# Kernel optimization log

Measured on AMD Instinct MI355X. Metric: run time of the kernel, lower is better.

Reference implementation:

```python
import jax, jax.numpy as jnp
import numpy as np

K = 1024          # num_embeddings (static for segment_sum)
D = 256           # embedding_dim
B, H, W = 32, 64, 64
DECAY = 0.99
EPS = 1e-05
BETA = 0.25


def setup_inputs() -> dict:
    key = jax.random.key(0)
    k1, k2 = jax.random.split(key)
    z = jax.random.normal(k1, (B, D, H, W), dtype=jnp.float32)
    embedding = jax.random.normal(k2, (K, D), dtype=jnp.float32)
    ema_cluster_size = jnp.zeros((K,), dtype=jnp.float32)
    ema_embedding = embedding.copy()
    return {"z": z, "embedding": embedding,
            "ema_cluster_size": ema_cluster_size,
            "ema_embedding": ema_embedding}


def reference(z, embedding, ema_cluster_size, ema_embedding):
    b, d, h, w = z.shape
    # (B, D, H, W) -> (B*H*W, D)
    z_flat = jnp.transpose(z, (0, 2, 3, 1)).reshape(-1, d)
    # squared L2 distances to each code: ||z||^2 - 2 z.E^T + ||E||^2  -> (N, K)
    dist = (jnp.sum(z_flat * z_flat, axis=1, keepdims=True)
            - 2.0 * (z_flat @ embedding.T)
            + jnp.sum(embedding * embedding, axis=1))
    encoding_indices = jnp.argmin(dist, axis=1)                 # (N,)
    # one-hot @ embedding == gather
    quantized = embedding[encoding_indices]                     # (N, D)
    quantized = jnp.transpose(quantized.reshape(b, h, w, d), (0, 3, 1, 2))
    # EMA buffer updates (encodings.sum(0) and encodings.T @ z_flat as segment sums)
    counts = jax.ops.segment_sum(jnp.ones_like(encoding_indices, dtype=z.dtype),
                                 encoding_indices, num_segments=K)
    dw = jax.ops.segment_sum(z_flat, encoding_indices, num_segments=K)
    new_cluster_size = DECAY * ema_cluster_size + (1.0 - DECAY) * counts
    new_ema_embedding = DECAY * ema_embedding + (1.0 - DECAY) * dw
    # straight-through estimator
    quantized_ste = z + jax.lax.stop_gradient(quantized - z)
    commitment_loss = BETA * jnp.mean(jnp.square(z - jax.lax.stop_gradient(quantized_ste)))
    return (quantized_ste, commitment_loss, encoding_indices,
            new_cluster_size, new_ema_embedding)
```

## Files before the change

### kernel.cpp

```cpp
#include <hip/hip_runtime.h>

#define KC 1024
#define DD 256
#define NP 131072
#define HWSZ 4096
#define TOTZ 33554432

#define OUT_Q    0
#define OUT_LOSS 33554432
#define OUT_IDX  33554433
#define OUT_CS   33685505
#define OUT_EMA  33686529

#define WS_IDX    0
#define WS_COUNTS 131072
#define WS_RCNT   132096
#define WS_LOSSP  132352
#define WS_ENORM  132608
#define WS_RLIST  133632
#define WS_EAUG   264704
#define WS_ZAUG   657920
#define WS_NEED_FLOATS (WS_ZAUG + 33554432)

#define MARGIN 0.0625f
#define RTILE 16

typedef __attribute__((ext_vector_type(8))) short bf16x8;
typedef __attribute__((ext_vector_type(4))) float f32x4;

__device__ inline unsigned short f2bf_rne(float x) {
    unsigned u = __float_as_uint(x);
    unsigned r = u + 0x7FFFu + ((u >> 16) & 1u);
    return (unsigned short)(r >> 16);
}
__device__ inline float bf2f(unsigned short h) {
    return __uint_as_float(((unsigned)h) << 16);
}
__device__ inline void gl_lds16(const void* g, void* l) {
    __builtin_amdgcn_global_load_lds(
        (const __attribute__((address_space(1))) unsigned int*)g,
        (__attribute__((address_space(3))) unsigned int*)l, 16, 0, 0);
}
__device__ inline unsigned long long packkey(float d, int c) {
    unsigned u = __float_as_uint(d);
    u = (u & 0x80000000u) ? ~u : (u | 0x80000000u);
    return (((unsigned long long)u) << 32) | (unsigned)c;
}

__global__ __launch_bounds__(256) void enorm_kernel(const float* __restrict__ emb,
                                                    float* __restrict__ enorm) {
    const int k = blockIdx.x;
    float v = emb[k * DD + threadIdx.x];
    v *= v;
    #pragma unroll
    for (int off = 32; off > 0; off >>= 1) v += __shfl_down(v, off);
    __shared__ float red[4];
    if ((threadIdx.x & 63) == 0) red[threadIdx.x >> 6] = v;
    __syncthreads();
    if (threadIdx.x == 0) enorm[k] = (red[0] + red[1]) + (red[2] + red[3]);
}

__global__ __launch_bounds__(256) void convert_z_kernel(
    const float* __restrict__ z, unsigned short* __restrict__ zaug)
{
    const int blk = blockIdx.x;
    const int pt = blk >> 2, kslot = blk & 3;
    const int kbase0 = kslot * 64;
    unsigned short* outH = zaug + (size_t)(pt * 8 + kslot) * 8192;
    unsigned short* outM = zaug + (size_t)(pt * 8 + 4 + kslot) * 8192;
    #pragma unroll
    for (int i = 0; i < 4; ++i) {
        const int f = i * 256 + threadIdx.x;
        const int kc = f >> 9, mt = (f >> 6) & 7, lane = f & 63;
        const int q = lane >> 4, col = lane & 15;
        const int p = pt * 128 + mt * 16 + col;
        const int b = p >> 12, hw = p & 4095;
        const int k0 = kbase0 + kc * 32 + q * 8;
        const float* src = z + (size_t)b * 1048576 + (size_t)k0 * 4096 + hw;
        unsigned short vh[8], vm[8];
        #pragma unroll
        for (int j = 0; j < 8; ++j) {
            const float x = src[j * 4096];
            const unsigned short h = f2bf_rne(x);
            vh[j] = h;
            vm[j] = f2bf_rne(x - bf2f(h));
        }
        *(uint4*)(outH + (size_t)f * 8) = *(uint4*)vh;
        *(uint4*)(outM + (size_t)f * 8) = *(uint4*)vm;
    }
}

__global__ __launch_bounds__(256) void convert_emb_kernel(
    const float* __restrict__ emb, unsigned short* __restrict__ eaug)
{
    const int blk = blockIdx.x;
    const int cc = blk / 12, ks = blk % 12;
    const int mode = (ks >= 8);
    unsigned short* outp = eaug + (size_t)blk * 8192;
    #pragma unroll
    for (int i = 0; i < 4; ++i) {
        const int f = i * 256 + threadIdx.x;
        const int kc = f >> 9, nt = (f >> 6) & 7, lane = f & 63;
        const int q = lane >> 4, col = lane & 15;
        const int n = cc * 128 + nt * 16 + col;
        const int k0 = ((ks * 64) & 255) + kc * 32 + q * 8;
        const float* src = emb + (size_t)n * 256 + k0;
        unsigned short v[8];
        #pragma unroll
        for (int j = 0; j < 8; ++j) {
            const float x = src[j];
            const unsigned short h = f2bf_rne(x);
            v[j] = mode ? f2bf_rne(x - bf2f(h)) : h;
        }
        *(uint4*)(outp + (size_t)f * 8) = *(uint4*)v;
    }
}

__global__ __launch_bounds__(512) void gemm_argmin_kernel(
    const unsigned short* __restrict__ zaug, const unsigned short* __restrict__ eaug,
    const float* __restrict__ enorm, int* __restrict__ idx_out,
    float* __restrict__ idx_out_f, float* __restrict__ counts,
    int* __restrict__ rcnt, int* __restrict__ rlist)
{
    __shared__ float smem[12288];
    unsigned short* aS   = (unsigned short*)smem;
    unsigned short* bAll = aS + 8192;
    const int t = threadIdx.x, w = t >> 6, lane = t & 63;
    const int w2 = w & 3, cho = w >> 2;
    const int mh = w2 & 1, nh = w2 >> 1;
    const int pt = blockIdx.x;

    const int aoff = w * 1024 + lane * 8;
    const int boff = w * 2048 + lane * 8;

    float rb[16], rs[16]; int ri[16];
    #pragma unroll
    for (int s = 0; s < 16; ++s) { rb[s] = 3.4e38f; rs[s] = 3.4e38f; ri[s] = 0; }

    #pragma unroll 1
    for (int pp = 0; pp < 4; ++pp) {
        const int cc = pp * 2 + cho;
        f32x4 acc[4][4];
        #pragma unroll
        for (int mi = 0; mi < 4; ++mi)
            #pragma unroll
            for (int ni = 0; ni < 4; ++ni) acc[mi][ni] = (f32x4){0.f, 0.f, 0.f, 0.f};

        float en[4];
        #pragma unroll
        for (int ni = 0; ni < 4; ++ni)
            en[ni] = enorm[cc * 128 + nh * 64 + ni * 16 + (lane & 15)];

        #pragma unroll 1
        for (int ks = 0; ks < 12; ++ks) {
            const int ksA = (ks < 8) ? ks : (ks - 8);
            const unsigned short* ga = zaug + ((size_t)(pt * 8 + ksA)) * 8192;
            const unsigned short* gbase = (w < 4)
                ? eaug + ((size_t)((pp * 2 + 0) * 12 + ks)) * 8192
                : eaug + ((size_t)((pp * 2 + 1) * 12 + ks)) * 8192 - 8192;
            __syncthreads();
            gl_lds16(ga + aoff, aS + aoff);
            gl_lds16(ga + aoff + 512, aS + aoff + 512);
            #pragma unroll
            for (int j = 0; j < 4; ++j)
                gl_lds16(gbase + boff + j * 512, bAll + boff + j * 512);
            __syncthreads();
            #pragma unroll
            for (int kc = 0; kc < 2; ++kc) {
                bf16x8 af[4], bf[4];
                #pragma unroll
                for (int mi = 0; mi < 4; ++mi)
                    af[mi] = *(const bf16x8*)(aS + kc * 4096 + (mh * 4 + mi) * 512 + lane * 8);
                #pragma unroll
                for (int ni = 0; ni < 4; ++ni)
                    bf[ni] = *(const bf16x8*)(bAll + cho * 8192 + kc * 4096 + (nh * 4 + ni) * 512 + lane * 8);
                #pragma unroll
                for (int mi = 0; mi < 4; ++mi)
                    #pragma unroll
                    for (int ni = 0; ni < 4; ++ni)
                        acc[mi][ni] = __builtin_amdgcn_mfma_f32_16x16x32_bf16(
                            af[mi], bf[ni], acc[mi][ni], 0, 0, 0);
            }
        }
        #pragma unroll
        for (int mi = 0; mi < 4; ++mi) {
            #pragma unroll
            for (int r = 0; r < 4; ++r) {
                const int s = mi * 4 + r;
                float v0 = fmaf(-2.f, acc[mi][0][r], en[0]);
                float v1 = fmaf(-2.f, acc[mi][1][r], en[1]);
                float v2 = fmaf(-2.f, acc[mi][2][r], en[2]);
                float v3 = fmaf(-2.f, acc[mi][3][r], en[3]);
                const int nb = cc * 128 + nh * 64 + (lane & 15);
                float b01 = fminf(v0, v1), x01 = fmaxf(v0, v1);
                int   i01 = (v1 < v0) ? nb + 16 : nb;
                float b23 = fminf(v2, v3), x23 = fmaxf(v2, v3);
                int   i23 = (v3 < v2) ? nb + 48 : nb + 32;
                float b = fminf(b01, b23);
                int   ib = (b23 < b01) ? i23 : i01;
                float s2 = fminf(fmaxf(b01, b23), fminf(x01, x23));
                if (b < rb[s]) { rs[s] = fminf(rb[s], s2); rb[s] = b; ri[s] = ib; }
                else           { rs[s] = fminf(rs[s], b); }
            }
        }
    }

    float B = 3.4e38f, S = 3.4e38f; int I = 0;
    const int mi_f = (t >> 4) & 3, q_f = (t >> 2) & 3, r_f = t & 3;
    const int s_f = mi_f * 4 + r_f;
    #pragma unroll 1
    for (int phase = 0; phase < 2; ++phase) {
        __syncthreads();
        if (cho == phase) {
            #pragma unroll
            for (int s = 0; s < 16; ++s) {
                smem[w2 * 1024 + s * 64 + lane] = rb[s];
                smem[4096 + w2 * 1024 + s * 64 + lane] = rs[s];
                ((int*)smem)[8192 + w2 * 1024 + s * 64 + lane] = ri[s];
            }
        }
        __syncthreads();
        if (t < 128) {
            #pragma unroll
            for (int hh = 0; hh < 2; ++hh) {
                const int wv = (t >> 6) + hh * 2;
                const int base = wv * 1024 + s_f * 64 + q_f * 16;
                #pragma unroll
                for (int ln = 0; ln < 16; ++ln) {
                    const float b = smem[base + ln];
                    const float s2 = smem[4096 + base + ln];
                    const int   i = ((int*)smem)[8192 + base + ln];
                    if (b < B) { S = fminf(B, s2); B = b; I = i; }
                    else       { S = fminf(S, b); }
                }
            }
        }
    }
    if (t < 128) {
        const int p = pt * 128 + t;
        idx_out[p] = I;
        idx_out_f[p] = (float)I;
        atomicAdd(&counts[I], 1.0f);
        if (S - B < MARGIN) {
            const int pos = atomicAdd(rcnt, 1);
            rlist[pos] = p;
        }
    }
}

__global__ __launch_bounds__(256) void rescue_kernel(
    const float* __restrict__ z, const float* __restrict__ emb,
    const float* __restrict__ enorm, const int* __restrict__ rcnt,
    const int* __restrict__ rlist, int* __restrict__ idx_out,
    float* __restrict__ idx_out_f, float* __restrict__ counts)
{
    __shared__ float zl[RTILE][DD];
    __shared__ unsigned long long lkey[RTILE];
    const int n = *rcnt;
    if (n <= 0) return;
    const int ntiles = (n + RTILE - 1) / RTILE;
    const int t = threadIdx.x;
    const int slot = t & 15, drow = t >> 4;
    #pragma unroll 1
    for (int tile = blockIdx.x; tile < ntiles; tile += gridDim.x) {
        const int base = tile * RTILE;
        {
            const int ridx = min(base + slot, n - 1);
            const int p = rlist[ridx];
            const int b = p >> 12, hw = p & 4095;
            const float* zp = z + (size_t)b * 1048576 + hw;
            #pragma unroll
            for (int j = 0; j < 16; ++j)
                zl[slot][drow * 16 + j] = zp[(size_t)(drow * 16 + j) * 4096];
        }
        if (t < RTILE) lkey[t] = ~0ull;
        __syncthreads();
        float dot[RTILE][4];
        #pragma unroll
        for (int p = 0; p < RTILE; ++p)
            #pragma unroll
            for (int ci = 0; ci < 4; ++ci) dot[p][ci] = 0.f;
        #pragma unroll 1
        for (int d4 = 0; d4 < 64; ++d4) {
            float4 ev[4];
            #pragma unroll
            for (int ci = 0; ci < 4; ++ci)
                ev[ci] = *(const float4*)(emb + (size_t)(ci * 256 + t) * 256 + d4 * 4);
            #pragma unroll
            for (int p = 0; p < RTILE; ++p) {
                const float4 zv = *(const float4*)(&zl[p][d4 * 4]);
                #pragma unroll
                for (int ci = 0; ci < 4; ++ci) {
                    dot[p][ci] = fmaf(zv.x, ev[ci].x, dot[p][ci]);
                    dot[p][ci] = fmaf(zv.y, ev[ci].y, dot[p][ci]);
                    dot[p][ci] = fmaf(zv.z, ev[ci].z, dot[p][ci]);
                    dot[p][ci] = fmaf(zv.w, ev[ci].w, dot[p][ci]);
                }
            }
        }
        float en[4];
        #pragma unroll
        for (int ci = 0; ci < 4; ++ci) en[ci] = enorm[ci * 256 + t];
        #pragma unroll
        for (int p = 0; p < RTILE; ++p) {
            unsigned long long k = packkey(fmaf(-2.f, dot[p][0], en[0]), t);
            #pragma unroll
            for (int ci = 1; ci < 4; ++ci) {
                const unsigned long long k2 =
                    packkey(fmaf(-2.f, dot[p][ci], en[ci]), ci * 256 + t);
                k = (k2 < k) ? k2 : k;
            }
            atomicMin(&lkey[p], k);
        }
        __syncthreads();
        if (t < RTILE && base + t < n) {
            const int p = rlist[base + t];
            const int fc = (int)(lkey[t] & 0xFFFFFFFFull);
            const int old = idx_out[p];
            if (fc != old) {
                atomicAdd(&counts[old], -1.0f);
                atomicAdd(&counts[fc], 1.0f);
                idx_out[p] = fc;
                idx_out_f[p] = (float)fc;
            }
        }
        __syncthreads();
    }
}

__global__ __launch_bounds__(512) void dwq_kernel(
    const float* __restrict__ z, const float* __restrict__ emb,
    const int* __restrict__ idx, const float* __restrict__ ema_emb,
    float* __restrict__ out_q, float* __restrict__ out_ema,
    float* __restrict__ lossp)
{
    __shared__ float kdw[KC];
    __shared__ float ecol[KC];
    __shared__ float red[8];
    const int d = blockIdx.x;
    const int t = threadIdx.x;
    #pragma unroll
    for (int k = t; k < KC; k += 512) { kdw[k] = 0.f; ecol[k] = emb[(size_t)k * 256 + d]; }
    __syncthreads();
    float ls = 0.f;
    #pragma unroll 1
    for (int it = 0; it < 64; ++it) {
        const int e = it * 512 + t;
        const int b = e >> 10, hwi = (e & 1023) << 2;
        const size_t zoff = (size_t)b * 1048576 + (size_t)d * 4096 + hwi;
        const float4 zv = *(const float4*)(z + zoff);
        const int4 iv = *(const int4*)(idx + b * 4096 + hwi);
        const float q0 = ecol[iv.x], q1 = ecol[iv.y], q2 = ecol[iv.z], q3 = ecol[iv.w];
        float4 qv; qv.x = q0; qv.y = q1; qv.z = q2; qv.w = q3;
        *(float4*)(out_q + zoff) = qv;
        atomicAdd(&kdw[iv.x], zv.x);
        atomicAdd(&kdw[iv.y], zv.y);
        atomicAdd(&kdw[iv.z], zv.z);
        atomicAdd(&kdw[iv.w], zv.w);
        const float d0 = zv.x - q0, d1 = zv.y - q1, d2 = zv.z - q2, d3 = zv.w - q3;
        ls += (d0 * d0 + d1 * d1) + (d2 * d2 + d3 * d3);
    }
    __syncthreads();
    #pragma unroll
    for (int k = t; k < KC; k += 512)
        out_ema[(size_t)k * 256 + d] = 0.99f * ema_emb[(size_t)k * 256 + d] + 0.01f * kdw[k];
    #pragma unroll
    for (int off = 32; off > 0; off >>= 1) ls += __shfl_down(ls, off);
    if ((t & 63) == 0) red[t >> 6] = ls;
    __syncthreads();
    if (t == 0) {
        float s = 0.f;
        #pragma unroll
        for (int i = 0; i < 8; ++i) s += red[i];
        lossp[blockIdx.x] = s;
    }
}

__global__ __launch_bounds__(256) void finalize_kernel(
    const float* __restrict__ ema_cs, const float* __restrict__ counts,
    const float* __restrict__ lossp, float* __restrict__ out)
{
    const int i = blockIdx.x * 256 + threadIdx.x;
    out[OUT_CS + i] = 0.99f * ema_cs[i] + 0.01f * counts[i];
    if (blockIdx.x == 0) {
        float s = lossp[threadIdx.x];
        #pragma unroll
        for (int off = 32; off > 0; off >>= 1) s += __shfl_down(s, off);
        __shared__ float red[4];
        if ((threadIdx.x & 63) == 0) red[threadIdx.x >> 6] = s;
        __syncthreads();
        if (threadIdx.x == 0)
            out[OUT_LOSS] = 0.25f * ((red[0] + red[1]) + (red[2] + red[3])) / 33554432.0f;
    }
}

__global__ __launch_bounds__(256) void dist_argmin_kernel(
    const float* __restrict__ z, const float* __restrict__ emb,
    const float* __restrict__ enorm, int* __restrict__ idx_out,
    float* __restrict__ idx_out_f, float* __restrict__ counts)
{
    __shared__ float smem[4096];
    float* As = smem;
    float* Bs = smem + 1024;
    const int tid = threadIdx.x;
    const int tx = tid & 15, ty = tid >> 4;
    const int p0 = blockIdx.x * 128;
    const int b = p0 >> 12, hw0 = p0 & 4095;
    const float* zb = z + (size_t)b * (DD * HWSZ) + hw0;
    const int arow = (tid & 31) * 4, akd = tid >> 5;
    const int bcode = tid >> 1, bj = (tid & 1) * 4;
    float best[8]; int bidx[8];
    #pragma unroll
    for (int i = 0; i < 8; i++) { best[i] = 3.4e38f; bidx[i] = 0; }
    #pragma unroll 1
    for (int cc = 0; cc < 8; ++cc) {
        const int c0 = cc * 128;
        float acc[8][8];
        #pragma unroll
        for (int i = 0; i < 8; i++)
            #pragma unroll
            for (int j = 0; j < 8; j++) acc[i][j] = 0.0f;
        #pragma unroll 1
        for (int dk = 0; dk < 32; ++dk) {
            const int kk0 = dk * 8;
            const float4 av = *(const float4*)(zb + (kk0 + akd) * HWSZ + arow);
            const float4 bv = *(const float4*)(emb + (c0 + bcode) * DD + kk0 + bj);
            __syncthreads();
            *(float4*)(As + akd * 128 + arow) = av;
            Bs[(bj + 0) * 128 + bcode] = bv.x;
            Bs[(bj + 1) * 128 + bcode] = bv.y;
            Bs[(bj + 2) * 128 + bcode] = bv.z;
            Bs[(bj + 3) * 128 + bcode] = bv.w;
            __syncthreads();
            #pragma unroll
            for (int kk = 0; kk < 8; ++kk) {
                const float4 a0 = *(const float4*)(As + kk * 128 + ty * 8);
                const float4 a1 = *(const float4*)(As + kk * 128 + ty * 8 + 4);
                const float4 b0 = *(const float4*)(Bs + kk * 128 + tx * 8);
                const float4 b1 = *(const float4*)(Bs + kk * 128 + tx * 8 + 4);
                const float a[8] = {a0.x,a0.y,a0.z,a0.w,a1.x,a1.y,a1.z,a1.w};
                const float bb[8] = {b0.x,b0.y,b0.z,b0.w,b1.x,b1.y,b1.z,b1.w};
                #pragma unroll
                for (int i = 0; i < 8; i++)
                    #pragma unroll
                    for (int j = 0; j < 8; j++)
                        acc[i][j] = fmaf(a[i], bb[j], acc[i][j]);
            }
        }
        const float4 en0 = *(const float4*)(enorm + c0 + tx * 8);
        const float4 en1 = *(const float4*)(enorm + c0 + tx * 8 + 4);
        const float en[8] = {en0.x,en0.y,en0.z,en0.w,en1.x,en1.y,en1.z,en1.w};
        #pragma unroll
        for (int j = 0; j < 8; j++) {
            const int c = c0 + tx * 8 + j;
            #pragma unroll
            for (int i = 0; i < 8; i++) {
                const float dist = fmaf(-2.0f, acc[i][j], en[j]);
                if (dist < best[i]) { best[i] = dist; bidx[i] = c; }
            }
        }
    }
    __syncthreads();
    float* rmin = smem;
    int* ridx = (int*)(smem + 2048);
    #pragma unroll
    for (int i = 0; i < 8; i++) {
        const int r = ty * 8 + i;
        rmin[r * 16 + tx] = best[i];
        ridx[r * 16 + tx] = bidx[i];
    }
    __syncthreads();
    if (tid < 128) {
        const int r = tid;
        float m = rmin[r * 16]; int mi = ridx[r * 16];
        #pragma unroll
        for (int tt = 1; tt < 16; tt++) {
            const float v = rmin[r * 16 + tt];
            const int vi = ridx[r * 16 + tt];
            if (v < m || (v == m && vi < mi)) { m = v; mi = vi; }
        }
        const int p = p0 + r;
        idx_out[p] = mi;
        idx_out_f[p] = (float)mi;
        atomicAdd(&counts[mi], 1.0f);
    }
}

extern "C" void kernel_launch(void* const* d_in, const int* in_sizes, int n_in,
                              void* d_out, int out_size, void* d_ws, size_t ws_size,
                              hipStream_t stream) {
    const float* z       = (const float*)d_in[0];
    const float* emb     = (const float*)d_in[1];
    const float* ema_cs  = (const float*)d_in[2];
    const float* ema_emb = (const float*)d_in[3];
    float* out = (float*)d_out;
    float* ws  = (float*)d_ws;

    int*   ws_idx    = (int*)(ws + WS_IDX);
    float* ws_counts = ws + WS_COUNTS;
    int*   ws_rcnt   = (int*)(ws + WS_RCNT);
    float* ws_lossp  = ws + WS_LOSSP;
    float* ws_enorm  = ws + WS_ENORM;
    int*   ws_rlist  = (int*)(ws + WS_RLIST);
    unsigned short* ws_eaug = (unsigned short*)(ws + WS_EAUG);
    unsigned short* ws_zaug = (unsigned short*)(ws + WS_ZAUG);

    hipMemsetAsync(ws_counts, 0, 1025 * sizeof(float), stream);
    hipLaunchKernelGGL(enorm_kernel, dim3(KC), dim3(256), 0, stream, emb, ws_enorm);

    if (ws_size >= (size_t)WS_NEED_FLOATS * sizeof(float)) {
        hipLaunchKernelGGL(convert_z_kernel, dim3(4096), dim3(256), 0, stream, z, ws_zaug);
        hipLaunchKernelGGL(convert_emb_kernel, dim3(96), dim3(256), 0, stream, emb, ws_eaug);
        hipLaunchKernelGGL(gemm_argmin_kernel, dim3(1024), dim3(512), 0, stream,
                           ws_zaug, ws_eaug, ws_enorm, ws_idx, out + OUT_IDX,
                           ws_counts, ws_rcnt, ws_rlist);
        hipLaunchKernelGGL(rescue_kernel, dim3(512), dim3(256), 0, stream,
                           z, emb, ws_enorm, ws_rcnt, ws_rlist,
                           ws_idx, out + OUT_IDX, ws_counts);
    } else {
        hipLaunchKernelGGL(dist_argmin_kernel, dim3(NP / 128), dim3(256), 0, stream,
                           z, emb, ws_enorm, ws_idx, out + OUT_IDX, ws_counts);
    }

    hipLaunchKernelGGL(dwq_kernel, dim3(DD), dim3(512), 0, stream,
                       z, emb, ws_idx, ema_emb, out, out + OUT_EMA, ws_lossp);
    hipLaunchKernelGGL(finalize_kernel, dim3(4), dim3(256), 0, stream,
                       ema_cs, ws_counts, ws_lossp, out);
}
```

Measured before the change: 863.3 us.

## Stage whole z tile in LDS and stream codebook fragments from global into registers

The GEMM-argmin kernel now loads the block's entire A (z) tile for each k-phase into a larger LDS buffer with only two barrier pairs per group. The embedding (B) fragments are read straight from global memory into registers, with the next k-step prefetched. This drops the per-k-step __syncthreads and the LDS staging of B. Waves are repartitioned so each covers an M half and an N quarter, and the final argmin reduction is split by M half. The cost is more LDS use, which may lower occupancy, and B fragments are fetched redundantly per wave from global or L2.

```diff
diff --git a/kernel.cpp b/kernel.cpp
--- a/kernel.cpp
+++ b/kernel.cpp
@@ -122,64 +122,85 @@
     float* __restrict__ idx_out_f, float* __restrict__ counts,
     int* __restrict__ rcnt, int* __restrict__ rlist)
 {
-    __shared__ float smem[12288];
-    unsigned short* aS   = (unsigned short*)smem;
-    unsigned short* bAll = aS + 8192;
+    __shared__ float smem[16384];
+    unsigned short* aS = (unsigned short*)smem;
     const int t = threadIdx.x, w = t >> 6, lane = t & 63;
-    const int w2 = w & 3, cho = w >> 2;
-    const int mh = w2 & 1, nh = w2 >> 1;
+    const int mh = w & 1, nq = w >> 1;
+    const int col = lane & 15;
     const int pt = blockIdx.x;
 
-    const int aoff = w * 1024 + lane * 8;
-    const int boff = w * 2048 + lane * 8;
-
     float rb[16], rs[16]; int ri[16];
     #pragma unroll
     for (int s = 0; s < 16; ++s) { rb[s] = 3.4e38f; rs[s] = 3.4e38f; ri[s] = 0; }
 
+    const unsigned short* zb = zaug + (size_t)pt * 65536;
+
     #pragma unroll 1
-    for (int pp = 0; pp < 4; ++pp) {
-        const int cc = pp * 2 + cho;
+    for (int g = 0; g < 4; ++g) {
+        const int ccg = g * 2 + (nq >> 1);
+        const int nbase = ccg * 128 + (nq & 1) * 64;
+        const unsigned short* eb = eaug + (size_t)ccg * (12 * 8192)
+                                 + (nq & 1) * 2048 + (size_t)lane * 8;
         f32x4 acc[4][4];
         #pragma unroll
         for (int mi = 0; mi < 4; ++mi)
             #pragma unroll
             for (int ni = 0; ni < 4; ++ni) acc[mi][ni] = (f32x4){0.f, 0.f, 0.f, 0.f};
-
         float en[4];
         #pragma unroll
-        for (int ni = 0; ni < 4; ++ni)
-            en[ni] = enorm[cc * 128 + nh * 64 + ni * 16 + (lane & 15)];
+        for (int ni = 0; ni < 4; ++ni) en[ni] = enorm[nbase + ni * 16 + col];
 
         #pragma unroll 1
-        for (int ks = 0; ks < 12; ++ks) {
-            const int ksA = (ks < 8) ? ks : (ks - 8);
-            const unsigned short* ga = zaug + ((size_t)(pt * 8 + ksA)) * 8192;
-            const unsigned short* gbase = (w < 4)
-                ? eaug + ((size_t)((pp * 2 + 0) * 12 + ks)) * 8192
-                : eaug + ((size_t)((pp * 2 + 1) * 12 + ks)) * 8192 - 8192;
+        for (int ph = 0; ph < 2; ++ph) {
             __syncthreads();
-            gl_lds16(ga + aoff, aS + aoff);
-            gl_lds16(ga + aoff + 512, aS + aoff + 512);
-            #pragma unroll
-            for (int j = 0; j < 4; ++j)
-                gl_lds16(gbase + boff + j * 512, bAll + boff + j * 512);
+            #pragma unroll
+            for (int i = 0; i < 8; ++i) {
+                const int off = i * 4096 + w * 512 + lane * 8;
+                gl_lds16(zb + ph * 32768 + off, aS + off);
+            }
             __syncthreads();
-            #pragma unroll
-            for (int kc = 0; kc < 2; ++kc) {
-                bf16x8 af[4], bf[4];
+            const int nks = ph ? 4 : 8;
+            bf16x8 bcur[2][4], bnxt[2][4];
+            {
+                const unsigned short* ebk = eb + (size_t)(ph ? 4 : 0) * 8192;
                 #pragma unroll
-                for (int mi = 0; mi < 4; ++mi)
-                    af[mi] = *(const bf16x8*)(aS + kc * 4096 + (mh * 4 + mi) * 512 + lane * 8);
-                #pragma unroll
-                for (int ni = 0; ni < 4; ++ni)
-                    bf[ni] = *(const bf16x8*)(bAll + cho * 8192 + kc * 4096 + (nh * 4 + ni) * 512 + lane * 8);
-                #pragma unroll
-                for (int mi = 0; mi < 4; ++mi)
+                for (int kc = 0; kc < 2; ++kc)
                     #pragma unroll
                     for (int ni = 0; ni < 4; ++ni)
-                        acc[mi][ni] = __builtin_amdgcn_mfma_f32_16x16x32_bf16(
-                            af[mi], bf[ni], acc[mi][ni], 0, 0, 0);
+                        bcur[kc][ni] = *(const bf16x8*)(ebk + kc * 4096 + ni * 512);
+            }
+            #pragma unroll 1
+            for (int j = 0; j < nks; ++j) {
+                const int slab = j & 3;
+                if (j + 1 < nks) {
+                    const int jn = j + 1;
+                    const int ksn = ph ? (4 + jn) : ((jn < 4) ? jn : jn + 4);
+                    const unsigned short* ebk = eb + (size_t)ksn * 8192;
+                    #pragma unroll
+                    for (int kc = 0; kc < 2; ++kc)
+                        #pragma unroll
+                        for (int ni = 0; ni < 4; ++ni)
+                            bnxt[kc][ni] = *(const bf16x8*)(ebk + kc * 4096 + ni * 512);
+                }
+                #pragma unroll
+                for (int kc = 0; kc < 2; ++kc) {
+                    bf16x8 af[4];
+                    #pragma unroll
+                    for (int mi = 0; mi < 4; ++mi)
+                        af[mi] = *(const bf16x8*)(aS + slab * 8192 + kc * 4096
+                                                  + (mh * 4 + mi) * 512 + lane * 8);
+                    #pragma unroll
+                    for (int mi = 0; mi < 4; ++mi)
+                        #pragma unroll
+                        for (int ni = 0; ni < 4; ++ni)
+                            acc[mi][ni] = __builtin_amdgcn_mfma_f32_16x16x32_bf16(
+                                af[mi], bcur[kc][ni], acc[mi][ni], 0, 0, 0);
+                }
+                #pragma unroll
+                for (int kc = 0; kc < 2; ++kc)
+                    #pragma unroll
+                    for (int ni = 0; ni < 4; ++ni)
+                        bcur[kc][ni] = bnxt[kc][ni];
             }
         }
         #pragma unroll
@@ -191,7 +212,7 @@
                 float v1 = fmaf(-2.f, acc[mi][1][r], en[1]);
                 float v2 = fmaf(-2.f, acc[mi][2][r], en[2]);
                 float v3 = fmaf(-2.f, acc[mi][3][r], en[3]);
-                const int nb = cc * 128 + nh * 64 + (lane & 15);
+                const int nb = nbase + col;
                 float b01 = fminf(v0, v1), x01 = fmaxf(v0, v1);
                 int   i01 = (v1 < v0) ? nb + 16 : nb;
                 float b23 = fminf(v2, v3), x23 = fmaxf(v2, v3);
@@ -205,45 +226,46 @@
         }
     }
 
-    float B = 3.4e38f, S = 3.4e38f; int I = 0;
-    const int mi_f = (t >> 4) & 3, q_f = (t >> 2) & 3, r_f = t & 3;
-    const int s_f = mi_f * 4 + r_f;
+    float* rbS = smem;
+    float* rsS = smem + 4096;
+    int*   riS = (int*)(smem + 8192);
     #pragma unroll 1
-    for (int phase = 0; phase < 2; ++phase) {
+    for (int ph = 0; ph < 2; ++ph) {
         __syncthreads();
-        if (cho == phase) {
+        if (mh == ph) {
             #pragma unroll
             for (int s = 0; s < 16; ++s) {
-                smem[w2 * 1024 + s * 64 + lane] = rb[s];
-                smem[4096 + w2 * 1024 + s * 64 + lane] = rs[s];
-                ((int*)smem)[8192 + w2 * 1024 + s * 64 + lane] = ri[s];
+                rbS[nq * 1024 + s * 64 + lane] = rb[s];
+                rsS[nq * 1024 + s * 64 + lane] = rs[s];
+                riS[nq * 1024 + s * 64 + lane] = ri[s];
             }
         }
         __syncthreads();
-        if (t < 128) {
-            #pragma unroll
-            for (int hh = 0; hh < 2; ++hh) {
-                const int wv = (t >> 6) + hh * 2;
-                const int base = wv * 1024 + s_f * 64 + q_f * 16;
+        if (t < 64) {
+            const int r = t;
+            const int mi = r >> 4, q = (r >> 2) & 3, rr = r & 3;
+            const int s = mi * 4 + rr;
+            float B = 3.4e38f, S = 3.4e38f; int I = 0;
+            #pragma unroll
+            for (int wv = 0; wv < 4; ++wv) {
+                const int base = wv * 1024 + s * 64 + q * 16;
                 #pragma unroll
                 for (int ln = 0; ln < 16; ++ln) {
-                    const float b = smem[base + ln];
-                    const float s2 = smem[4096 + base + ln];
-                    const int   i = ((int*)smem)[8192 + base + ln];
+                    const float b = rbS[base + ln];
+                    const float s2 = rsS[base + ln];
+                    const int   i = riS[base + ln];
                     if (b < B) { S = fminf(B, s2); B = b; I = i; }
                     else       { S = fminf(S, b); }
                 }
             }
-        }
-    }
-    if (t < 128) {
-        const int p = pt * 128 + t;
-        idx_out[p] = I;
-        idx_out_f[p] = (float)I;
-        atomicAdd(&counts[I], 1.0f);
-        if (S - B < MARGIN) {
-            const int pos = atomicAdd(rcnt, 1);
-            rlist[pos] = p;
+            const int p = pt * 128 + ph * 64 + r;
+            idx_out[p] = I;
+            idx_out_f[p] = (float)I;
+            atomicAdd(&counts[I], 1.0f);
+            if (S - B < MARGIN) {
+                const int pos = atomicAdd(rcnt, 1);
+                rlist[pos] = p;
+            }
         }
     }
 }
```

Result: faster. 826.8 us (-4.2%).
